# Kernel tuning notes

Hardware: AMD Instinct MI355X
Metric: run time of the kernel (lower is better)

## Reference

```python
import jax, jax.numpy as jnp
import numpy as np

N, D, E, K = 65536, 2048, 64, 8
EPS = 1e-5


def setup_inputs() -> dict:
    key = jax.random.key(0)
    kx, kw = jax.random.split(key)
    x = jax.random.normal(kx, (N, D), dtype=jnp.float32)
    # nn.Linear(input_size, num_experts, bias=False) weight: [E, D]
    W = jax.random.normal(kw, (E, D), dtype=jnp.float32) * (1.0 / np.sqrt(D))
    return {"x": x, "W": W}


def _l1_normalize(v):
    # torch F.normalize(p=1, dim=0): v / max(||v||_1, 1e-12)
    return v / jnp.maximum(jnp.sum(jnp.abs(v)), 1e-12)


def reference(x, W):
    # router logits: [N, E] in float32 (matches .float() in torch code)
    logits = (x @ W.T).astype(jnp.float32)
    top_v, top_i = jax.lax.top_k(logits, K)            # [N, K]
    top_k_gates = jax.nn.softmax(top_v, axis=-1).astype(x.dtype)
    # training-branch aux loss (compute_aux_loss)
    probs = jax.nn.softmax(logits, axis=-1)            # [N, E]
    rows = jnp.arange(logits.shape[0])[:, None]
    dense_gates = jnp.zeros_like(probs, dtype=top_k_gates.dtype).at[rows, top_i].set(top_k_gates)
    probs_sum = probs.sum(0)                           # [E]
    freq = (dense_gates > 0).astype(jnp.float32).sum(0)  # [E]
    # log(sum(exp(logits)) + eps)^2 summed, computed stably
    lse = jnp.logaddexp(jax.scipy.special.logsumexp(logits, axis=-1), jnp.log(EPS))
    zloss = jnp.sum(lse ** 2) / logits.shape[0]
    switchloss = E * jnp.sum(_l1_normalize(probs_sum) * _l1_normalize(freq))
    loss = switchloss + 0.1 * zloss
    return top_i, top_k_gates, loss
```

## Files before the change

### kernel.cpp

```cpp
#include <hip/hip_runtime.h>
#include <math.h>

#define NROWS 65536
#define DDIM 2048
#define NEXP 64
#define TOPK 8

constexpr int BM = 128;
constexpr int BK = 32;
constexpr int NTH = 256;
constexpr int NSTEP = DDIM / BK;
constexpr int CAP = 8192;
constexpr float THR = 3e-4f;

typedef short bf16x8 __attribute__((ext_vector_type(8)));
typedef float f32x4 __attribute__((ext_vector_type(4)));

__device__ inline unsigned short bfround(float f) {
    union { float f; unsigned u; } v; v.f = f;
    unsigned r = (v.u + 0x7fffu + ((v.u >> 16) & 1u)) >> 16;
    return (unsigned short)r;
}
__device__ inline float bf2f(unsigned short h) {
    union { unsigned u; float f; } v; v.u = ((unsigned)h) << 16;
    return v.f;
}
__device__ inline void cvt8(const float4& A, const float4& B, bf16x8& h, bf16x8& l) {
    float f[8] = {A.x, A.y, A.z, A.w, B.x, B.y, B.z, B.w};
#pragma unroll
    for (int j = 0; j < 8; ++j) {
        unsigned short hh = bfround(f[j]);
        h[j] = (short)hh;
        l[j] = (short)bfround(f[j] - bf2f(hh));
    }
}

__global__ __launch_bounds__(NTH, 1)
void gate_kernel(const float* __restrict__ x, const float* __restrict__ W,
                 float* __restrict__ out_idx, float* __restrict__ out_gate,
                 float* __restrict__ g_psum, float* __restrict__ g_freq,
                 float* __restrict__ g_zsum, int* __restrict__ g_cnt,
                 int* __restrict__ g_rows)
{
    __shared__ __align__(16) short Bfrag[2][2][4][64][8];
    __shared__ float psum_s[NEXP];
    __shared__ float fcnt_s[NEXP];

    const int tid = threadIdx.x;
    const int w = tid >> 6;
    const int lane = tid & 63;
    const int g = lane >> 4;
    const int c = lane & 15;
    const int row0 = blockIdx.x * BM + w * 32;

    if (tid < NEXP) { psum_s[tid] = 0.f; fcnt_s[tid] = 0.f; }

    const int se = tid >> 2;
    const int skg = tid & 3;
    const int sct = se >> 4;
    const int slane = (se & 15) + (skg << 4);

    const float* xr0 = x + (size_t)(row0 + c) * DDIM + g * 8;
    const float* xr1 = x + (size_t)(row0 + 16 + c) * DDIM + g * 8;
    const float* wp  = W + (size_t)se * DDIM + skg * 8;

    f32x4 acc[2][4];
#pragma unroll
    for (int rt = 0; rt < 2; ++rt)
#pragma unroll
        for (int ct = 0; ct < 4; ++ct) acc[rt][ct] = (f32x4){0.f, 0.f, 0.f, 0.f};

    float4 xa[2][2], xb[2][2];

    auto stageB = [&](int k0, int buf) {
        float4 a = *reinterpret_cast<const float4*>(wp + k0);
        float4 b = *reinterpret_cast<const float4*>(wp + k0 + 4);
        bf16x8 h, l;
        cvt8(a, b, h, l);
        *reinterpret_cast<bf16x8*>(&Bfrag[buf][0][sct][slane][0]) = h;
        *reinterpret_cast<bf16x8*>(&Bfrag[buf][1][sct][slane][0]) = l;
    };

    xa[0][0] = *reinterpret_cast<const float4*>(xr0);
    xa[0][1] = *reinterpret_cast<const float4*>(xr0 + 4);
    xa[1][0] = *reinterpret_cast<const float4*>(xr1);
    xa[1][1] = *reinterpret_cast<const float4*>(xr1 + 4);
    stageB(0, 0);
    __syncthreads();

    for (int t = 0; t < NSTEP; ++t) {
        const int buf = t & 1;
        const int kn = (t + 1) * BK;
        if (t + 1 < NSTEP) {
            xb[0][0] = *reinterpret_cast<const float4*>(xr0 + kn);
            xb[0][1] = *reinterpret_cast<const float4*>(xr0 + kn + 4);
            xb[1][0] = *reinterpret_cast<const float4*>(xr1 + kn);
            xb[1][1] = *reinterpret_cast<const float4*>(xr1 + kn + 4);
            stageB(kn, buf ^ 1);
        }
        bf16x8 ah[2], al[2];
        cvt8(xa[0][0], xa[0][1], ah[0], al[0]);
        cvt8(xa[1][0], xa[1][1], ah[1], al[1]);
        bf16x8 bh[4], bl[4];
#pragma unroll
        for (int ct = 0; ct < 4; ++ct) {
            bh[ct] = *reinterpret_cast<const bf16x8*>(&Bfrag[buf][0][ct][lane][0]);
            bl[ct] = *reinterpret_cast<const bf16x8*>(&Bfrag[buf][1][ct][lane][0]);
        }
#pragma unroll
        for (int rt = 0; rt < 2; ++rt)
#pragma unroll
            for (int ct = 0; ct < 4; ++ct) {
                acc[rt][ct] = __builtin_amdgcn_mfma_f32_16x16x32_bf16(
                    ah[rt], bh[ct], acc[rt][ct], 0, 0, 0);
                acc[rt][ct] = __builtin_amdgcn_mfma_f32_16x16x32_bf16(
                    ah[rt], bl[ct], acc[rt][ct], 0, 0, 0);
                acc[rt][ct] = __builtin_amdgcn_mfma_f32_16x16x32_bf16(
                    al[rt], bh[ct], acc[rt][ct], 0, 0, 0);
            }
#pragma unroll
        for (int rt = 0; rt < 2; ++rt)
#pragma unroll
            for (int i = 0; i < 2; ++i) xa[rt][i] = xb[rt][i];
        __syncthreads();
    }

    float pcol[4] = {0.f, 0.f, 0.f, 0.f};
    float zsq_acc = 0.f;

#pragma unroll
    for (int rt = 0; rt < 2; ++rt) {
#pragma unroll
        for (int reg = 0; reg < 4; ++reg) {
            const int row = row0 + rt * 16 + g * 4 + reg;
            float ld[4];
#pragma unroll
            for (int ct = 0; ct < 4; ++ct) ld[ct] = acc[rt][ct][reg];

            float tv[9]; int ti[9];
#pragma unroll
            for (int p = 0; p < 9; ++p) {
                float bv = -3.4e38f; int bgi = 127;
#pragma unroll
                for (int ct = 0; ct < 4; ++ct) {
                    int e = ct * 16 + c;
                    if (ld[ct] > bv) { bv = ld[ct]; bgi = e; }
                }
#pragma unroll
                for (int m = 1; m < 16; m <<= 1) {
                    float ov = __shfl_xor(bv, m, 16);
                    int ogi = __shfl_xor(bgi, m, 16);
                    if (ov > bv || (ov == bv && ogi < bgi)) { bv = ov; bgi = ogi; }
                }
                tv[p] = bv; ti[p] = bgi;
#pragma unroll
                for (int ct = 0; ct < 4; ++ct)
                    if (bgi == ct * 16 + c) ld[ct] = -3.4e38f;
            }

            float mg = 3.4e38f;
#pragma unroll
            for (int p = 0; p < 8; ++p) mg = fminf(mg, tv[p] - tv[p + 1]);
            if (c == 0 && mg < THR) {
                int idx = atomicAdd(g_cnt, 1);
                if (idx < CAP) g_rows[idx] = row;
            }

            const float m0 = tv[0];
            float pe[4], ps = 0.f;
#pragma unroll
            for (int ct = 0; ct < 4; ++ct) {
                pe[ct] = expf(acc[rt][ct][reg] - m0);
                ps += pe[ct];
            }
            float s = ps;
#pragma unroll
            for (int m = 1; m < 16; m <<= 1) s += __shfl_xor(s, m, 16);
            const float inv_s = 1.f / s;
#pragma unroll
            for (int ct = 0; ct < 4; ++ct) pcol[ct] += pe[ct] * inv_s;

            if (c == 0) {
                float lsef = m0 + logf(s);
                const float lb = -11.512925464970229f;
                float mx = fmaxf(lsef, lb), mn = fminf(lsef, lb);
                float z = mx + log1pf(expf(mn - mx));
                zsq_acc += z * z;
            }

            float gs = 0.f;
#pragma unroll
            for (int p = 0; p < 8; ++p) gs += expf(tv[p] - m0);
            if (c < 8) {
                float mytv = tv[0]; int myti = ti[0];
#pragma unroll
                for (int p = 1; p < 8; ++p)
                    if (c == p) { mytv = tv[p]; myti = ti[p]; }
                const size_t base = (size_t)row * TOPK;
                out_idx[base + c] = (float)myti;
                out_gate[base + c] = expf(mytv - m0) / gs;
                atomicAdd(&fcnt_s[myti], 1.f);
            }
        }
    }

#pragma unroll
    for (int off = 32; off > 0; off >>= 1) zsq_acc += __shfl_down(zsq_acc, off, 64);
    if (lane == 0) atomicAdd(g_zsum, zsq_acc);

#pragma unroll
    for (int ct = 0; ct < 4; ++ct) atomicAdd(&psum_s[ct * 16 + c], pcol[ct]);
    __syncthreads();
    if (tid < NEXP) {
        atomicAdd(&g_psum[tid], psum_s[tid]);
        atomicAdd(&g_freq[tid], fcnt_s[tid]);
    }
}

__global__ __launch_bounds__(256, 1)
void fixup_kernel(const float* __restrict__ x, const float* __restrict__ W,
                  float* __restrict__ out_idx, float* __restrict__ out_gate,
                  const int* __restrict__ g_cnt, const int* __restrict__ g_rows)
{
    const int n = min(*g_cnt, CAP);
    const int tid = threadIdx.x;
    const int e = tid >> 2;
    const int q = tid & 3;
    __shared__ double sL[NEXP];

    for (int i = blockIdx.x; i < n; i += gridDim.x) {
        const int row = g_rows[i];
        const float* xr = x + (size_t)row * DDIM;
        const float* wr = W + (size_t)e * DDIM;

        double p0 = 0.0, p1 = 0.0, p2 = 0.0, p3 = 0.0;
#pragma unroll 4
        for (int j = 0; j < DDIM / 16; ++j) {
            const int k = j * 16 + q * 4;
            float4 wv = *reinterpret_cast<const float4*>(wr + k);
            float4 xv = *reinterpret_cast<const float4*>(xr + k);
            p0 = fma((double)xv.x, (double)wv.x, p0);
            p1 = fma((double)xv.y, (double)wv.y, p1);
            p2 = fma((double)xv.z, (double)wv.z, p2);
            p3 = fma((double)xv.w, (double)wv.w, p3);
        }
        double s = (p0 + p1) + (p2 + p3);
        s += __shfl_xor(s, 1, 4);
        s += __shfl_xor(s, 2, 4);
        if (q == 0) sL[e] = s;
        __syncthreads();

        if (tid < NEXP) {
            const int lane = tid;
            double v = sL[lane];
            double tv[8]; int ti[8];
#pragma unroll
            for (int p = 0; p < 8; ++p) {
                double bv = v; int bgi = lane;
#pragma unroll
                for (int m = 1; m < 64; m <<= 1) {
                    double ov = __shfl_xor(bv, m, 64);
                    int ogi = __shfl_xor(bgi, m, 64);
                    if (ov > bv || (ov == bv && ogi < bgi)) { bv = ov; bgi = ogi; }
                }
                tv[p] = bv; ti[p] = bgi;
                if (lane == bgi) v = -HUGE_VAL;
            }

            const double m0 = tv[0];
            double gs = 0.0, ge[8];
#pragma unroll
            for (int j = 0; j < 8; ++j) { ge[j] = exp(tv[j] - m0); gs += ge[j]; }
            if (lane < 8) {
                double myge = ge[0]; int myti = ti[0];
#pragma unroll
                for (int j = 1; j < 8; ++j)
                    if (lane == j) { myge = ge[j]; myti = ti[j]; }
                const size_t base = (size_t)row * TOPK;
                out_idx[base + lane] = (float)myti;
                out_gate[base + lane] = (float)(myge / gs);
            }
        }
        __syncthreads();
    }
}

__global__ void finalize_kernel(const float* __restrict__ g_psum,
                                const float* __restrict__ g_freq,
                                const float* __restrict__ g_zsum,
                                float* __restrict__ out_loss)
{
    const int lane = threadIdx.x & 63;
    float p = g_psum[lane], f = g_freq[lane];
    float sp = p, sf = f;
#pragma unroll
    for (int m = 1; m < 64; m <<= 1) { sp += __shfl_xor(sp, m, 64); sf += __shfl_xor(sf, m, 64); }
    sp = fmaxf(sp, 1e-12f);
    sf = fmaxf(sf, 1e-12f);
    float term = (p / sp) * (f / sf);
#pragma unroll
    for (int m = 1; m < 64; m <<= 1) term += __shfl_xor(term, m, 64);
    if (lane == 0)
        out_loss[0] = (float)NEXP * term + 0.1f * (g_zsum[0] / (float)NROWS);
}

extern "C" void kernel_launch(void* const* d_in, const int* in_sizes, int n_in,
                              void* d_out, int out_size, void* d_ws, size_t ws_size,
                              hipStream_t stream)
{
    const float* x = (const float*)d_in[0];
    const float* W = (const float*)d_in[1];
    float* out = (float*)d_out;
    float* out_idx  = out;
    float* out_gate = out + (size_t)NROWS * TOPK;
    float* out_loss = out + (size_t)2 * NROWS * TOPK;

    float* acc = (float*)d_ws;
    int* cnt  = (int*)d_ws + 129;
    int* rows = (int*)d_ws + 130;
    hipMemsetAsync(d_ws, 0, 130 * sizeof(float), stream);

    gate_kernel<<<NROWS / BM, NTH, 0, stream>>>(
        x, W, out_idx, out_gate, acc, acc + NEXP, acc + 2 * NEXP, cnt, rows);
    fixup_kernel<<<2048, 256, 0, stream>>>(x, W, out_idx, out_gate, cnt, rows);
    finalize_kernel<<<1, 64, 0, stream>>>(acc, acc + NEXP, acc + 2 * NEXP, out_loss);
}
```

Measured before the change: 251.0 us.

## Recompute only near-tie candidate experts in fixup using stored approximate logits

The main kernel now also stores the approximate logits of each ambiguous row into workspace. The fixup kernel reads them, picks only the experts within a threshold of the 9th-largest value (at most 16), and recomputes those dot products in double precision instead of all 64. This cuts fixup work and reads of W and x by several times per ambiguous row. It adds extra workspace writes in the main kernel, and correctness now relies on the candidate threshold capturing every expert that could change the top-k.

```diff
diff --git a/kernel.cpp b/kernel.cpp
--- a/kernel.cpp
+++ b/kernel.cpp
@@ -40,7 +40,7 @@
                  float* __restrict__ out_idx, float* __restrict__ out_gate,
                  float* __restrict__ g_psum, float* __restrict__ g_freq,
                  float* __restrict__ g_zsum, int* __restrict__ g_cnt,
-                 int* __restrict__ g_rows)
+                 int* __restrict__ g_rows, float* __restrict__ g_logits)
 {
     __shared__ __align__(16) short Bfrag[2][2][4][64][8];
     __shared__ float psum_s[NEXP];
@@ -161,9 +161,16 @@
             float mg = 3.4e38f;
 #pragma unroll
             for (int p = 0; p < 8; ++p) mg = fminf(mg, tv[p] - tv[p + 1]);
-            if (c == 0 && mg < THR) {
-                int idx = atomicAdd(g_cnt, 1);
-                if (idx < CAP) g_rows[idx] = row;
+            if (mg < THR) {
+                int idx = 0;
+                if (c == 0) idx = atomicAdd(g_cnt, 1);
+                idx = __shfl(idx, (lane >> 4) << 4, 64);
+                if (idx < CAP) {
+                    if (c == 0) g_rows[idx] = row;
+#pragma unroll
+                    for (int ct = 0; ct < 4; ++ct)
+                        g_logits[(size_t)idx * NEXP + ct * 16 + c] = acc[rt][ct][reg];
+                }
             }
 
             const float m0 = tv[0];
@@ -220,43 +227,81 @@
 __global__ __launch_bounds__(256, 1)
 void fixup_kernel(const float* __restrict__ x, const float* __restrict__ W,
                   float* __restrict__ out_idx, float* __restrict__ out_gate,
-                  const int* __restrict__ g_cnt, const int* __restrict__ g_rows)
+                  const int* __restrict__ g_cnt, const int* __restrict__ g_rows,
+                  const float* __restrict__ g_logits)
 {
     const int n = min(*g_cnt, CAP);
     const int tid = threadIdx.x;
-    const int e = tid >> 2;
-    const int q = tid & 3;
-    __shared__ double sL[NEXP];
+    const int grp = tid >> 5;
+    const int gl = tid & 31;
+    __shared__ float sLog[NEXP];
+    __shared__ double sD[16];
+    __shared__ int sCand[16];
+    __shared__ int sNc;
 
     for (int i = blockIdx.x; i < n; i += gridDim.x) {
         const int row = g_rows[i];
-        const float* xr = x + (size_t)row * DDIM;
-        const float* wr = W + (size_t)e * DDIM;
-
-        double p0 = 0.0, p1 = 0.0, p2 = 0.0, p3 = 0.0;
-#pragma unroll 4
-        for (int j = 0; j < DDIM / 16; ++j) {
-            const int k = j * 16 + q * 4;
-            float4 wv = *reinterpret_cast<const float4*>(wr + k);
-            float4 xv = *reinterpret_cast<const float4*>(xr + k);
-            p0 = fma((double)xv.x, (double)wv.x, p0);
-            p1 = fma((double)xv.y, (double)wv.y, p1);
-            p2 = fma((double)xv.z, (double)wv.z, p2);
-            p3 = fma((double)xv.w, (double)wv.w, p3);
-        }
-        double s = (p0 + p1) + (p2 + p3);
-        s += __shfl_xor(s, 1, 4);
-        s += __shfl_xor(s, 2, 4);
-        if (q == 0) sL[e] = s;
+        if (tid < NEXP) sLog[tid] = g_logits[(size_t)i * NEXP + tid];
+        if (tid == 0) sNc = 0;
         __syncthreads();
 
         if (tid < NEXP) {
             const int lane = tid;
-            double v = sL[lane];
+            const float myv = sLog[lane];
+            float vv = myv;
+            float v9 = 0.f;
+#pragma unroll
+            for (int p = 0; p < 9; ++p) {
+                float bv = vv; int bgi = lane;
+#pragma unroll
+                for (int m = 1; m < 64; m <<= 1) {
+                    float ov = __shfl_xor(bv, m, 64);
+                    int ogi = __shfl_xor(bgi, m, 64);
+                    if (ov > bv || (ov == bv && ogi < bgi)) { bv = ov; bgi = ogi; }
+                }
+                if (lane == bgi) vv = -3.4e38f;
+                v9 = bv;
+            }
+            if (myv >= v9 - THR) {
+                int slot = atomicAdd(&sNc, 1);
+                if (slot < 16) sCand[slot] = lane;
+            }
+        }
+        __syncthreads();
+        const int nc = min(sNc, 16);
+
+        const float* xr = x + (size_t)row * DDIM;
+        for (int cb = 0; cb < nc; cb += 8) {
+            const int ci = cb + grp;
+            if (ci < nc) {
+                const float* wr = W + (size_t)sCand[ci] * DDIM;
+                double p0 = 0.0, p1 = 0.0, p2 = 0.0, p3 = 0.0;
+#pragma unroll
+                for (int j = 0; j < 16; ++j) {
+                    const int k = j * 128 + gl * 4;
+                    float4 wv = *reinterpret_cast<const float4*>(wr + k);
+                    float4 xv = *reinterpret_cast<const float4*>(xr + k);
+                    p0 = fma((double)xv.x, (double)wv.x, p0);
+                    p1 = fma((double)xv.y, (double)wv.y, p1);
+                    p2 = fma((double)xv.z, (double)wv.z, p2);
+                    p3 = fma((double)xv.w, (double)wv.w, p3);
+                }
+                double s = (p0 + p1) + (p2 + p3);
+#pragma unroll
+                for (int m = 1; m < 32; m <<= 1) s += __shfl_xor(s, m, 32);
+                if (gl == 0) sD[ci] = s;
+            }
+        }
+        __syncthreads();
+
+        if (tid < NEXP) {
+            const int lane = tid;
+            double v = (lane < nc) ? sD[lane] : -HUGE_VAL;
+            int id = (lane < nc) ? sCand[lane] : 1000;
             double tv[8]; int ti[8];
 #pragma unroll
             for (int p = 0; p < 8; ++p) {
-                double bv = v; int bgi = lane;
+                double bv = v; int bgi = id;
 #pragma unroll
                 for (int m = 1; m < 64; m <<= 1) {
                     double ov = __shfl_xor(bv, m, 64);
@@ -264,7 +309,7 @@
                     if (ov > bv || (ov == bv && ogi < bgi)) { bv = ov; bgi = ogi; }
                 }
                 tv[p] = bv; ti[p] = bgi;
-                if (lane == bgi) v = -HUGE_VAL;
+                if (id == bgi) v = -HUGE_VAL;
             }
 
             const double m0 = tv[0];
@@ -315,13 +360,14 @@
     float* out_gate = out + (size_t)NROWS * TOPK;
     float* out_loss = out + (size_t)2 * NROWS * TOPK;
 
-    float* acc = (float*)d_ws;
-    int* cnt  = (int*)d_ws + 129;
-    int* rows = (int*)d_ws + 130;
+    float* acc    = (float*)d_ws;
+    int*   cnt    = (int*)d_ws + 129;
+    int*   rows   = (int*)d_ws + 130;
+    float* logits = (float*)d_ws + 130 + CAP;
     hipMemsetAsync(d_ws, 0, 130 * sizeof(float), stream);
 
     gate_kernel<<<NROWS / BM, NTH, 0, stream>>>(
-        x, W, out_idx, out_gate, acc, acc + NEXP, acc + 2 * NEXP, cnt, rows);
-    fixup_kernel<<<2048, 256, 0, stream>>>(x, W, out_idx, out_gate, cnt, rows);
+        x, W, out_idx, out_gate, acc, acc + NEXP, acc + 2 * NEXP, cnt, rows, logits);
+    fixup_kernel<<<2048, 256, 0, stream>>>(x, W, out_idx, out_gate, cnt, rows, logits);
     finalize_kernel<<<1, 64, 0, stream>>>(acc, acc + NEXP, acc + 2 * NEXP, out_loss);
 }
```

Measured after the change: 237.5 us. 1.06x faster.
